# Optimization experiments

Hardware: AMD Instinct MI355X
Metric: run time of the kernel (lower is better)

## Reference

```python
import jax, jax.numpy as jnp
import numpy as np

B, S, D, H, DFF = 4, 2048, 768, 12, 3072
DH = D // H  # 64
EPS = 1e-5
SQRT_DK = float(np.sqrt(DH))


def layer_norm(x, gamma, beta):
    mu = jnp.mean(x, axis=-1, keepdims=True)
    var = jnp.mean((x - mu) ** 2, axis=-1, keepdims=True)
    return (x - mu) / jnp.sqrt(var + EPS) * gamma + beta


def attention_block(x, Wq, Wv, gamma, beta, mask):
    # NOTE: faithful to source quirks: k and v BOTH come from the V projection
    # (self.K is unused), and softmax is over dim=2 (the QUERY axis) as in
    # nn.Softmax(dim=2) applied to a (B, H, Sq, Sk) tensor.
    b, s, d = x.shape
    q = (x @ Wq).reshape(b, s, H, DH).transpose(0, 2, 1, 3)   # (B,H,S,DH)
    kv = (x @ Wv).reshape(b, s, H, DH).transpose(0, 2, 1, 3)  # (B,H,S,DH)
    w = jnp.einsum('bhqd,bhkd->bhqk', q, kv) / SQRT_DK        # (B,H,S,S)
    w = jnp.where(mask, -1e9, w)
    score = jax.nn.softmax(w, axis=2)  # dim=2 quirk (query axis)
    o = jnp.einsum('bhqk,bhkd->bhqd', score, kv)
    o = o.transpose(0, 2, 1, 3).reshape(b, s, d)
    return layer_norm(o + x, gamma, beta)


def feed_forward(x, W1, b1, W2, b2, gamma, beta):
    h = jax.nn.relu(x @ W1 + b1)
    return layer_norm(h @ W2 + b2 + x, gamma, beta)


def setup_inputs() -> dict:
    key = jax.random.key(0)
    ks = jax.random.split(key, 12)
    std = 1.0 / np.sqrt(D)
    x = jax.random.normal(ks[0], (B, S, D), dtype=jnp.float32)
    # causal mask: True = masked
    mask = jnp.triu(jnp.ones((S, S), dtype=bool), k=1)[None, None]
    return {
        'x': x,
        'mask': mask,
        'Wq1': jax.random.normal(ks[1], (D, D), jnp.float32) * std,
        'Wv1': jax.random.normal(ks[2], (D, D), jnp.float32) * std,
        'g1': jnp.ones((D,), jnp.float32),
        'be1': jnp.zeros((D,), jnp.float32),
        'Wq2': jax.random.normal(ks[3], (D, D), jnp.float32) * std,
        'Wv2': jax.random.normal(ks[4], (D, D), jnp.float32) * std,
        'g2': jnp.ones((D,), jnp.float32),
        'be2': jnp.zeros((D,), jnp.float32),
        'Wf1': jax.random.normal(ks[5], (D, DFF), jnp.float32) * std,
        'bf1': jnp.zeros((DFF,), jnp.float32),
        'Wf2': jax.random.normal(ks[6], (DFF, D), jnp.float32) * (1.0 / np.sqrt(DFF)),
        'bf2': jnp.zeros((D,), jnp.float32),
        'gf': jnp.ones((D,), jnp.float32),
        'bef': jnp.zeros((D,), jnp.float32),
    }


def reference(x, mask, Wq1, Wv1, g1, be1, Wq2, Wv2, g2, be2,
              Wf1, bf1, Wf2, bf2, gf, bef):
    x = attention_block(x, Wq1, Wv1, g1, be1, mask)
    # second block: mask is zeroed in the source (no masking)
    x = attention_block(x, Wq2, Wv2, g2, be2, jnp.zeros_like(mask))
    x = feed_forward(x, Wf1, bf1, Wf2, bf2, gf, bef)
    return x
```

## Files before the change

### kernel.cpp

```cpp
#include <hip/hip_runtime.h>

typedef __attribute__((ext_vector_type(8))) short short8;
typedef __attribute__((ext_vector_type(4))) float floatx4;
typedef __attribute__((ext_vector_type(4))) unsigned short ushort4v;

#define H_ 12
#define S_ 2048
#define D_ 768
#define DFF_ 3072
#define DH_ 64
#define BH_ 48
#define M_ 8192

__device__ __forceinline__ unsigned short f2bf(float f) {
  union { float f; unsigned int u; } a; a.f = f;
  return (unsigned short)((a.u + 0x7FFFu + ((a.u >> 16) & 1u)) >> 16);
}

__device__ __forceinline__ void glds16(const void* g, void* l) {
  __builtin_amdgcn_global_load_lds(
      (const __attribute__((address_space(1))) void*)(unsigned long long)(size_t)g,
      (__attribute__((address_space(3))) void*)(unsigned int)(size_t)l, 16, 0, 0);
}
__device__ __forceinline__ void glds4(const void* g, void* l) {
  __builtin_amdgcn_global_load_lds(
      (const __attribute__((address_space(1))) void*)(unsigned long long)(size_t)g,
      (__attribute__((address_space(3))) void*)(unsigned int)(size_t)l, 4, 0, 0);
}

__device__ __forceinline__ int swz8(int lin, int nwg) {
  return (lin & 7) * (nwg >> 3) + (lin >> 3);
}

__global__ __launch_bounds__(256) void cvt_bf16(const float* __restrict__ in,
                                                unsigned short* __restrict__ out) {
  size_t i = ((size_t)blockIdx.x * 256 + threadIdx.x) * 4;
  floatx4 v = *reinterpret_cast<const floatx4*>(in + i);
  ushort4v o;
  o[0] = f2bf(v[0]); o[1] = f2bf(v[1]); o[2] = f2bf(v[2]); o[3] = f2bf(v[3]);
  *reinterpret_cast<ushort4v*>(out + i) = o;
}

__global__ __launch_bounds__(256) void wtrans(const float* __restrict__ W,
                                              unsigned short* __restrict__ Wt,
                                              int K, int N) {
  __shared__ float t[64][65];
  const int n0 = blockIdx.x * 64, k0 = blockIdx.y * 64;
  const int tid = threadIdx.x;
#pragma unroll
  for (int i = 0; i < 16; ++i) {
    int idx = tid + 256 * i;
    int kl = idx >> 6, nl = idx & 63;
    t[kl][nl] = W[(size_t)(k0 + kl) * N + n0 + nl];
  }
  __syncthreads();
#pragma unroll
  for (int i = 0; i < 16; ++i) {
    int idx = tid + 256 * i;
    int nl = idx >> 6, kl = idx & 63;
    Wt[(size_t)(n0 + nl) * K + k0 + kl] = f2bf(t[kl][nl]);
  }
}

__global__ __launch_bounds__(256) void kvtrans(const unsigned short* __restrict__ KVb,
                                               unsigned short* __restrict__ KVTb) {
  __shared__ unsigned short t[64][72];
  const int kk0 = blockIdx.x * 64;
  const int bh = blockIdx.y, b = bh / H_, h = bh % H_;
  const size_t xbase = ((size_t)b * S_) * D_ + h * DH_;
  const int tid = threadIdx.x;
#pragma unroll
  for (int i = 0; i < 16; ++i) {
    int idx = tid + 256 * i;
    int kl = idx >> 6, d = idx & 63;
    t[kl][d] = KVb[xbase + (size_t)(kk0 + kl) * D_ + d];
  }
  __syncthreads();
  const size_t tb = (size_t)bh * DH_ * S_;
#pragma unroll
  for (int i = 0; i < 16; ++i) {
    int idx = tid + 256 * i;
    int d = idx >> 6, kl = idx & 63;
    KVTb[tb + (size_t)d * S_ + kk0 + kl] = t[kl][d];
  }
}

template <int EPI, int OUTBF>
__global__ __launch_bounds__(256, 2) void gemm128(const unsigned short* __restrict__ A,
                                                  const unsigned short* __restrict__ Bt,
                                                  const float* __restrict__ bias,
                                                  float scale, void* __restrict__ C0,
                                                  void* __restrict__ C1,
                                                  int M, int N, int K, int lda) {
  __shared__ unsigned short As[128 * 64];
  __shared__ unsigned short Bs[128 * 64];
  const int tid = threadIdx.x;
  const int l = tid & 63, w = tid >> 6;
  const int wm = w >> 1, wn = w & 1;
  const int lrow = l & 15, lk = l >> 4;
  int lin = (blockIdx.z * gridDim.y + blockIdx.y) * gridDim.x + blockIdx.x;
  int nwg = gridDim.x * gridDim.y * gridDim.z;
  int s = swz8(lin, nwg);
  int xt = s % gridDim.x;
  int rest = s / gridDim.x;
  int yt = rest % gridDim.y;
  int zt = rest / gridDim.y;
  const unsigned short* Ao = A + (size_t)zt * K;
  const unsigned short* Bo = Bt + (size_t)zt * K;
  const int m0 = yt * 128, n0 = xt * 128;
  floatx4 acc[4][4] = {};
  for (int k0 = 0; k0 < K; k0 += 64) {
    __syncthreads();
#pragma unroll
    for (int i = 0; i < 4; ++i) {
      int idx = w * 64 + i * 256 + l;
      int row = idx >> 3, c8 = idx & 7;
      int sc = (c8 ^ (row & 7)) << 3;
      glds16(Ao + (size_t)(m0 + row) * lda + k0 + sc, As + (size_t)(w * 64 + i * 256) * 8);
      glds16(Bo + (size_t)(n0 + row) * lda + k0 + sc, Bs + (size_t)(w * 64 + i * 256) * 8);
    }
    __syncthreads();
#pragma unroll
    for (int ks = 0; ks < 2; ++ks) {
      short8 af[4], bfr[4];
#pragma unroll
      for (int f = 0; f < 4; ++f) {
        int ar = wm * 64 + f * 16 + lrow;
        af[f] = *reinterpret_cast<const short8*>(
            &As[ar * 64 + (((ks * 4 + lk) ^ (ar & 7)) << 3)]);
        int br = wn * 64 + f * 16 + lrow;
        bfr[f] = *reinterpret_cast<const short8*>(
            &Bs[br * 64 + (((ks * 4 + lk) ^ (br & 7)) << 3)]);
      }
#pragma unroll
      for (int fm = 0; fm < 4; ++fm)
#pragma unroll
        for (int fn = 0; fn < 4; ++fn)
          acc[fm][fn] =
              __builtin_amdgcn_mfma_f32_16x16x32_bf16(af[fm], bfr[fn], acc[fm][fn], 0, 0, 0);
    }
  }
#pragma unroll
  for (int fm = 0; fm < 4; ++fm) {
#pragma unroll
    for (int fn = 0; fn < 4; ++fn) {
      int col = n0 + wn * 64 + fn * 16 + lrow;
#pragma unroll
      for (int r = 0; r < 4; ++r) {
        int row = m0 + wm * 64 + fm * 16 + lk * 4 + r;
        float v = acc[fm][fn][r];
        if (EPI == 3) {
          if (col < 768)
            ((unsigned short*)C0)[(size_t)row * 768 + col] = f2bf(v * scale);
          else
            ((unsigned short*)C1)[(size_t)row * 768 + col - 768] = f2bf(v);
        } else {
          v = v * scale + ((EPI > 0) ? bias[col] : 0.0f);
          if (EPI == 1) v = fmaxf(v, 0.0f);
          void* Cz = zt ? C1 : C0;
          if (OUTBF) ((unsigned short*)Cz)[(size_t)row * N + col] = f2bf(v);
          else ((float*)Cz)[(size_t)row * N + col] = v;
        }
      }
    }
  }
}

template <bool CAUSAL>
__global__ __launch_bounds__(256, 4) void colsum(const unsigned short* __restrict__ Qb,
                                                 const unsigned short* __restrict__ KVb,
                                                 float* __restrict__ lnl) {
  __shared__ unsigned short kvs[64 * 64];
  __shared__ float lred[4][64];
  const int tid = threadIdx.x;
  const int l = tid & 63, w = tid >> 6;
  const int lrow = l & 15, lk = l >> 4;
  const int sw = swz8(blockIdx.x, 32 * BH_);
  const int bh = sw >> 5, kt = sw & 31;
  const int kk0 = kt * 64;
  const int b = bh / H_, h = bh % H_;
  const size_t xbase = ((size_t)b * S_) * D_ + h * DH_;
#pragma unroll
  for (int i = 0; i < 2; ++i) {
    int idx = w * 64 + i * 256 + l;
    int row = idx >> 3, c8 = idx & 7;
    glds16(KVb + xbase + (size_t)(kk0 + row) * D_ + ((c8 ^ (row & 7)) << 3),
           kvs + (size_t)(w * 64 + i * 256) * 8);
  }
  __syncthreads();
  short8 bkv[4][2];
#pragma unroll
  for (int kkf = 0; kkf < 4; ++kkf)
#pragma unroll
    for (int s = 0; s < 2; ++s) {
      int br = kkf * 16 + lrow;
      bkv[kkf][s] = *reinterpret_cast<const short8*>(
          &kvs[br * 64 + (((s * 4 + lk) ^ (br & 7)) << 3)]);
    }
  float lrun[4] = {0.0f, 0.0f, 0.0f, 0.0f};
  const int qbase = CAUSAL ? kk0 : 0;
  const int ntiles = (S_ - qbase) >> 4;
  for (int t = w; t < ntiles; t += 4) {
    const int q0 = qbase + t * 16;
    const bool maskt = CAUSAL && (q0 < kk0 + 64);
    short8 aq[2];
#pragma unroll
    for (int s = 0; s < 2; ++s)
      aq[s] = *reinterpret_cast<const short8*>(
          &Qb[xbase + (size_t)(q0 + lrow) * D_ + s * 32 + lk * 8]);
#pragma unroll
    for (int kkf = 0; kkf < 4; ++kkf) {
      floatx4 sf = {};
      sf = __builtin_amdgcn_mfma_f32_16x16x32_bf16(aq[0], bkv[kkf][0], sf, 0, 0, 0);
      sf = __builtin_amdgcn_mfma_f32_16x16x32_bf16(aq[1], bkv[kkf][1], sf, 0, 0, 0);
      const int kkg = kk0 + kkf * 16 + lrow;
      float lacc = 0.0f;
      if (maskt) {
#pragma unroll
        for (int r = 0; r < 4; ++r) {
          int qg = q0 + lk * 4 + r;
          lacc += (kkg <= qg) ? __expf(sf[r]) : 0.0f;
        }
      } else {
#pragma unroll
        for (int r = 0; r < 4; ++r) lacc += __expf(sf[r]);
      }
      lrun[kkf] += lacc;
    }
  }
#pragma unroll
  for (int kkf = 0; kkf < 4; ++kkf) {
    float lv = lrun[kkf];
    lv += __shfl_xor(lv, 16, 64);
    lv += __shfl_xor(lv, 32, 64);
    if (l < 16) lred[w][kkf * 16 + l] = lv;
  }
  __syncthreads();
  if (tid < 64) {
    float lv = lred[0][tid] + lred[1][tid] + lred[2][tid] + lred[3][tid];
    lnl[(size_t)bh * S_ + kk0 + tid] = __logf(lv);
  }
}

template <bool CAUSAL>
__global__ __launch_bounds__(256, 3) void attnpv(const unsigned short* __restrict__ Qb,
                                                 const unsigned short* __restrict__ KVb,
                                                 const unsigned short* __restrict__ KVTb,
                                                 const float* __restrict__ lnl,
                                                 float* __restrict__ Opre) {
  __shared__ unsigned short kvs[2][64 * 64];
  __shared__ unsigned short kvts[2][64 * 64];
  __shared__ float slnl[2][4][64];
  __shared__ unsigned short ps[4][32 * 64];
  const int tid = threadIdx.x;
  const int l = tid & 63, w = tid >> 6;
  const int lrow = l & 15, lk = l >> 4;
  const int sw = swz8(blockIdx.x, 16 * BH_);
  const int bh = sw >> 4, qtr = sw & 15;
  const int qt = CAUSAL ? (15 - qtr) : qtr;
  const int q0 = qt * 128;
  const int wr = w * 32;
  const int b = bh / H_, h = bh % H_;
  const size_t xbase = ((size_t)b * S_) * D_ + h * DH_;
  const size_t tbase = (size_t)bh * DH_ * S_;
  const float* lnlb = lnl + (size_t)bh * S_;

  auto STAGE = [&](int buf, int t) {
    const int kk0 = t * 64;
#pragma unroll
    for (int i = 0; i < 2; ++i) {
      int idx = w * 64 + i * 256 + l;
      int row = idx >> 3, c8 = idx & 7;
      int sc = (c8 ^ (row & 7)) << 3;
      glds16(KVb + xbase + (size_t)(kk0 + row) * D_ + sc,
             &kvs[buf][(size_t)(w * 64 + i * 256) * 8]);
      glds16(KVTb + tbase + (size_t)row * S_ + kk0 + sc,
             &kvts[buf][(size_t)(w * 64 + i * 256) * 8]);
    }
    glds4(lnlb + kk0 + l, &slnl[buf][w][0]);
  };

  short8 aq[2][2];
#pragma unroll
  for (int fm = 0; fm < 2; ++fm)
#pragma unroll
    for (int s = 0; s < 2; ++s)
      aq[fm][s] = *reinterpret_cast<const short8*>(
          &Qb[xbase + (size_t)(q0 + wr + fm * 16 + lrow) * D_ + s * 32 + lk * 8]);
  floatx4 ao[2][4] = {};
  const int nkk = CAUSAL ? 2 * (qt + 1) : (S_ / 64);

  STAGE(0, 0);
  int cur = 0;
  for (int t = 0; t < nkk; ++t) {
    const int kk0 = t * 64;
    const bool maskt = CAUSAL && (kk0 + 64 > q0);
    if (t + 1 < nkk) {
      STAGE(cur ^ 1, t + 1);
      __builtin_amdgcn_sched_barrier(0);
      asm volatile("s_waitcnt vmcnt(5)" ::: "memory");
    } else {
      __builtin_amdgcn_sched_barrier(0);
      asm volatile("s_waitcnt vmcnt(0)" ::: "memory");
    }
    __builtin_amdgcn_s_barrier();
    __builtin_amdgcn_sched_barrier(0);
#pragma unroll
    for (int kkf = 0; kkf < 4; ++kkf) {
      const int kkl = kkf * 16 + lrow;
      const int br = kkf * 16 + lrow;
      short8 b0 =
          *reinterpret_cast<const short8*>(&kvs[cur][br * 64 + ((lk ^ (br & 7)) << 3)]);
      short8 b1 =
          *reinterpret_cast<const short8*>(&kvs[cur][br * 64 + (((4 + lk) ^ (br & 7)) << 3)]);
      const float nl = -slnl[cur][w][kkl];
      const int kkg = kk0 + kkl;
#pragma unroll
      for (int fm = 0; fm < 2; ++fm) {
        floatx4 sf = {nl, nl, nl, nl};
        sf = __builtin_amdgcn_mfma_f32_16x16x32_bf16(aq[fm][0], b0, sf, 0, 0, 0);
        sf = __builtin_amdgcn_mfma_f32_16x16x32_bf16(aq[fm][1], b1, sf, 0, 0, 0);
#pragma unroll
        for (int r = 0; r < 4; ++r) {
          int prow = fm * 16 + lk * 4 + r;
          float p;
          if (maskt)
            p = (kkg <= q0 + wr + prow) ? __expf(sf[r]) : 0.0f;
          else
            p = __expf(sf[r]);
          ps[w][prow * 64 + (((kkl >> 3) ^ (prow & 7)) << 3) + (kkl & 7)] = f2bf(p);
        }
      }
    }
    short8 pa[2][2];
#pragma unroll
    for (int fm = 0; fm < 2; ++fm)
#pragma unroll
      for (int s2 = 0; s2 < 2; ++s2)
        pa[fm][s2] = *reinterpret_cast<const short8*>(
            &ps[w][(fm * 16 + lrow) * 64 + (((s2 * 4 + lk) ^ (lrow & 7)) << 3)]);
    __builtin_amdgcn_s_setprio(1);
#pragma unroll
    for (int dn = 0; dn < 4; ++dn) {
#pragma unroll
      for (int s2 = 0; s2 < 2; ++s2) {
        const int br2 = dn * 16 + lrow;
        short8 bv = *reinterpret_cast<const short8*>(
            &kvts[cur][br2 * 64 + (((s2 * 4 + lk) ^ (br2 & 7)) << 3)]);
#pragma unroll
        for (int fm = 0; fm < 2; ++fm)
          ao[fm][dn] =
              __builtin_amdgcn_mfma_f32_16x16x32_bf16(pa[fm][s2], bv, ao[fm][dn], 0, 0, 0);
      }
    }
    __builtin_amdgcn_s_setprio(0);
    __builtin_amdgcn_sched_barrier(0);
    __builtin_amdgcn_s_barrier();
    __builtin_amdgcn_sched_barrier(0);
    cur ^= 1;
  }
#pragma unroll
  for (int fm = 0; fm < 2; ++fm)
#pragma unroll
    for (int dn = 0; dn < 4; ++dn)
#pragma unroll
      for (int r = 0; r < 4; ++r)
        Opre[xbase + (size_t)(q0 + wr + fm * 16 + lk * 4 + r) * D_ + dn * 16 + lrow] =
            ao[fm][dn][r];
}

template <bool WRITEBF, bool TWO, bool BIAS>
__global__ __launch_bounds__(256) void ln_kernel(const float* __restrict__ pre,
                                                 const float* __restrict__ pre2,
                                                 const float* __restrict__ bias,
                                                 const float* __restrict__ res,
                                                 const float* __restrict__ gam,
                                                 const float* __restrict__ bet,
                                                 float* __restrict__ outf,
                                                 unsigned short* __restrict__ outb) {
  __shared__ float red[8];
  const int tid = threadIdx.x;
  const size_t base = (size_t)blockIdx.x * D_;
  float v[3];
  float s = 0.0f;
#pragma unroll
  for (int j = 0; j < 3; ++j) {
    int i = tid + 256 * j;
    float t = pre[base + i] + res[base + i];
    if (TWO) t += pre2[base + i];
    if (BIAS) t += bias[i];
    v[j] = t;
    s += t;
  }
#pragma unroll
  for (int off = 32; off; off >>= 1) s += __shfl_xor(s, off, 64);
  if ((tid & 63) == 0) red[tid >> 6] = s;
  __syncthreads();
  s = red[0] + red[1] + red[2] + red[3];
  const float mu = s * (1.0f / 768.0f);
  float vs = 0.0f;
#pragma unroll
  for (int j = 0; j < 3; ++j) { float d = v[j] - mu; vs += d * d; }
#pragma unroll
  for (int off = 32; off; off >>= 1) vs += __shfl_xor(vs, off, 64);
  if ((tid & 63) == 0) red[4 + (tid >> 6)] = vs;
  __syncthreads();
  vs = red[4] + red[5] + red[6] + red[7];
  const float rstd = rsqrtf(vs * (1.0f / 768.0f) + 1e-5f);
#pragma unroll
  for (int j = 0; j < 3; ++j) {
    int i = tid + 256 * j;
    float o = (v[j] - mu) * rstd * gam[i] + bet[i];
    outf[base + i] = o;
    if (WRITEBF) outb[base + i] = f2bf(o);
  }
}

extern "C" void kernel_launch(void* const* d_in, const int* in_sizes, int n_in,
                              void* d_out, int out_size, void* d_ws, size_t ws_size,
                              hipStream_t stream) {
  const float* x = (const float*)d_in[0];
  const float* Wq1 = (const float*)d_in[2];
  const float* Wv1 = (const float*)d_in[3];
  const float* g1 = (const float*)d_in[4];
  const float* be1 = (const float*)d_in[5];
  const float* Wq2 = (const float*)d_in[6];
  const float* Wv2 = (const float*)d_in[7];
  const float* g2 = (const float*)d_in[8];
  const float* be2 = (const float*)d_in[9];
  const float* Wf1 = (const float*)d_in[10];
  const float* bf1 = (const float*)d_in[11];
  const float* Wf2 = (const float*)d_in[12];
  const float* bf2 = (const float*)d_in[13];
  const float* gf = (const float*)d_in[14];
  const float* bef = (const float*)d_in[15];

  char* ws = (char*)d_ws;
  size_t off = 0;
  auto alloc = [&](size_t bytes) -> void* {
    void* p = ws + off;
    off += (bytes + 255) & ~(size_t)255;
    return p;
  };
  unsigned short* xb = (unsigned short*)alloc((size_t)M_ * D_ * 2);
  unsigned short* qb = (unsigned short*)alloc((size_t)M_ * D_ * 2);
  unsigned short* kvb = (unsigned short*)alloc((size_t)M_ * D_ * 2);
  unsigned short* kvtb = (unsigned short*)alloc((size_t)BH_ * DH_ * S_ * 2);
  float* lnl = (float*)alloc((size_t)BH_ * S_ * 4);
  float* preA = (float*)alloc((size_t)M_ * D_ * 4);
  float* xcur = (float*)alloc((size_t)M_ * D_ * 4);
  unsigned short* hb = (unsigned short*)alloc((size_t)M_ * DFF_ * 2);
  unsigned short* wqv1t = (unsigned short*)alloc((size_t)D_ * 1536 * 2);
  unsigned short* wqv2t = (unsigned short*)alloc((size_t)D_ * 1536 * 2);
  unsigned short* wf1t = (unsigned short*)alloc((size_t)D_ * DFF_ * 2);
  unsigned short* wf2t = (unsigned short*)alloc((size_t)D_ * DFF_ * 2);
  float* preB = (float*)qb;
  if (off > ws_size) return;

  const dim3 blk(256);
  cvt_bf16<<<dim3((M_ * D_) / 1024), blk, 0, stream>>>(x, xb);
  wtrans<<<dim3(12, 12), blk, 0, stream>>>(Wq1, wqv1t, D_, D_);
  wtrans<<<dim3(12, 12), blk, 0, stream>>>(Wv1, wqv1t + (size_t)768 * 768, D_, D_);
  wtrans<<<dim3(12, 12), blk, 0, stream>>>(Wq2, wqv2t, D_, D_);
  wtrans<<<dim3(12, 12), blk, 0, stream>>>(Wv2, wqv2t + (size_t)768 * 768, D_, D_);
  wtrans<<<dim3(48, 12), blk, 0, stream>>>(Wf1, wf1t, D_, DFF_);
  wtrans<<<dim3(12, 48), blk, 0, stream>>>(Wf2, wf2t, DFF_, D_);

  const dim3 gqkv(12, 64);
  const dim3 gkvt(S_ / 64, BH_);

  gemm128<3, 1><<<gqkv, blk, 0, stream>>>(xb, wqv1t, nullptr, 0.125f, qb, kvb, M_, 1536, D_, D_);
  kvtrans<<<gkvt, blk, 0, stream>>>(kvb, kvtb);
  colsum<true><<<dim3(32 * BH_), blk, 0, stream>>>(qb, kvb, lnl);
  attnpv<true><<<dim3(16 * BH_), blk, 0, stream>>>(qb, kvb, kvtb, lnl, preA);
  ln_kernel<true, false, false><<<dim3(M_), blk, 0, stream>>>(preA, nullptr, nullptr, x, g1,
                                                              be1, xcur, xb);

  gemm128<3, 1><<<gqkv, blk, 0, stream>>>(xb, wqv2t, nullptr, 0.125f, qb, kvb, M_, 1536, D_, D_);
  kvtrans<<<gkvt, blk, 0, stream>>>(kvb, kvtb);
  colsum<false><<<dim3(32 * BH_), blk, 0, stream>>>(qb, kvb, lnl);
  attnpv<false><<<dim3(16 * BH_), blk, 0, stream>>>(qb, kvb, kvtb, lnl, preA);
  ln_kernel<true, false, false><<<dim3(M_), blk, 0, stream>>>(preA, nullptr, nullptr, xcur, g2,
                                                              be2, xcur, xb);

  gemm128<1, 1><<<dim3(24, 64), blk, 0, stream>>>(xb, wf1t, bf1, 1.0f, hb, nullptr, M_, DFF_,
                                                  D_, D_);
  gemm128<0, 0><<<dim3(6, 64, 2), blk, 0, stream>>>(hb, wf2t, nullptr, 1.0f, preA, preB, M_, D_,
                                                    DFF_ / 2, DFF_);
  ln_kernel<false, true, true><<<dim3(M_), blk, 0, stream>>>(preA, preB, bf2, xcur, gf, bef,
                                                             (float*)d_out, nullptr);
}
```

Baseline: 516.8 us.

## Use exp2 softmax with folded log2e, packed bf16 P stores, prefetch Q, one-wave LayerNorm

The Q scale now folds in log2(e) so the softmax kernels use exp2 and log2 hardware intrinsics instead of expf and logf. The stored log normalizer is negated, so attnpv can load it as a float4 accumulator init. attnpv swaps the MFMA operand order so each lane holds four consecutive keys, which lets the P tile be written to LDS with packed v_cvt_pk_bf16 32-bit stores. colsum software-prefetches the next Q tile. LayerNorm is rewritten to one wavefront per row with float4 loads and no LDS or barriers.

```diff
diff --git a/kernel.cpp b/kernel.cpp
--- a/kernel.cpp
+++ b/kernel.cpp
@@ -11,10 +11,31 @@
 #define DH_ 64
 #define BH_ 48
 #define M_ 8192
+#define QSCALE 0.180336880f
+
+#if defined(__has_builtin)
+#if __has_builtin(__builtin_amdgcn_exp2f)
+#define EXP2V(x) __builtin_amdgcn_exp2f(x)
+#endif
+#if __has_builtin(__builtin_amdgcn_logf)
+#define LOG2V(x) __builtin_amdgcn_logf(x)
+#endif
+#endif
+#ifndef EXP2V
+#define EXP2V(x) exp2f(x)
+#endif
+#ifndef LOG2V
+#define LOG2V(x) log2f(x)
+#endif
 
 __device__ __forceinline__ unsigned short f2bf(float f) {
   union { float f; unsigned int u; } a; a.f = f;
   return (unsigned short)((a.u + 0x7FFFu + ((a.u >> 16) & 1u)) >> 16);
+}
+__device__ __forceinline__ unsigned int cvtpk_bf16(float lo, float hi) {
+  unsigned int u;
+  asm("v_cvt_pk_bf16_f32 %0, %1, %2" : "=v"(u) : "v"(lo), "v"(hi));
+  return u;
 }
 
 __device__ __forceinline__ void glds16(const void* g, void* l) {
@@ -200,30 +221,41 @@
   float lrun[4] = {0.0f, 0.0f, 0.0f, 0.0f};
   const int qbase = CAUSAL ? kk0 : 0;
   const int ntiles = (S_ - qbase) >> 4;
+  short8 aqn[2];
+  if (w < ntiles) {
+    const int q0 = qbase + w * 16;
+#pragma unroll
+    for (int s = 0; s < 2; ++s)
+      aqn[s] = *reinterpret_cast<const short8*>(
+          &Qb[xbase + (size_t)(q0 + lrow) * D_ + s * 32 + lk * 8]);
+  }
   for (int t = w; t < ntiles; t += 4) {
     const int q0 = qbase + t * 16;
     const bool maskt = CAUSAL && (q0 < kk0 + 64);
-    short8 aq[2];
-#pragma unroll
-    for (int s = 0; s < 2; ++s)
-      aq[s] = *reinterpret_cast<const short8*>(
-          &Qb[xbase + (size_t)(q0 + lrow) * D_ + s * 32 + lk * 8]);
+    short8 aq0 = aqn[0], aq1 = aqn[1];
+    if (t + 4 < ntiles) {
+      const int qn = qbase + (t + 4) * 16;
+#pragma unroll
+      for (int s = 0; s < 2; ++s)
+        aqn[s] = *reinterpret_cast<const short8*>(
+            &Qb[xbase + (size_t)(qn + lrow) * D_ + s * 32 + lk * 8]);
+    }
 #pragma unroll
     for (int kkf = 0; kkf < 4; ++kkf) {
       floatx4 sf = {};
-      sf = __builtin_amdgcn_mfma_f32_16x16x32_bf16(aq[0], bkv[kkf][0], sf, 0, 0, 0);
-      sf = __builtin_amdgcn_mfma_f32_16x16x32_bf16(aq[1], bkv[kkf][1], sf, 0, 0, 0);
+      sf = __builtin_amdgcn_mfma_f32_16x16x32_bf16(aq0, bkv[kkf][0], sf, 0, 0, 0);
+      sf = __builtin_amdgcn_mfma_f32_16x16x32_bf16(aq1, bkv[kkf][1], sf, 0, 0, 0);
       const int kkg = kk0 + kkf * 16 + lrow;
       float lacc = 0.0f;
       if (maskt) {
 #pragma unroll
         for (int r = 0; r < 4; ++r) {
           int qg = q0 + lk * 4 + r;
-          lacc += (kkg <= qg) ? __expf(sf[r]) : 0.0f;
+          lacc += (kkg <= qg) ? EXP2V(sf[r]) : 0.0f;
         }
       } else {
 #pragma unroll
-        for (int r = 0; r < 4; ++r) lacc += __expf(sf[r]);
+        for (int r = 0; r < 4; ++r) lacc += EXP2V(sf[r]);
       }
       lrun[kkf] += lacc;
     }
@@ -238,7 +270,7 @@
   __syncthreads();
   if (tid < 64) {
     float lv = lred[0][tid] + lred[1][tid] + lred[2][tid] + lred[3][tid];
-    lnl[(size_t)bh * S_ + kk0 + tid] = __logf(lv);
+    lnl[(size_t)bh * S_ + kk0 + tid] = -LOG2V(lv);
   }
 }
 
@@ -307,29 +339,38 @@
     __builtin_amdgcn_sched_barrier(0);
 #pragma unroll
     for (int kkf = 0; kkf < 4; ++kkf) {
-      const int kkl = kkf * 16 + lrow;
       const int br = kkf * 16 + lrow;
       short8 b0 =
           *reinterpret_cast<const short8*>(&kvs[cur][br * 64 + ((lk ^ (br & 7)) << 3)]);
       short8 b1 =
           *reinterpret_cast<const short8*>(&kvs[cur][br * 64 + (((4 + lk) ^ (br & 7)) << 3)]);
-      const float nl = -slnl[cur][w][kkl];
-      const int kkg = kk0 + kkl;
+      const floatx4 nl4 =
+          *reinterpret_cast<const floatx4*>(&slnl[cur][w][kkf * 16 + lk * 4]);
+      const int kkbase = kk0 + kkf * 16 + lk * 4;
 #pragma unroll
       for (int fm = 0; fm < 2; ++fm) {
-        floatx4 sf = {nl, nl, nl, nl};
-        sf = __builtin_amdgcn_mfma_f32_16x16x32_bf16(aq[fm][0], b0, sf, 0, 0, 0);
-        sf = __builtin_amdgcn_mfma_f32_16x16x32_bf16(aq[fm][1], b1, sf, 0, 0, 0);
-#pragma unroll
-        for (int r = 0; r < 4; ++r) {
-          int prow = fm * 16 + lk * 4 + r;
-          float p;
-          if (maskt)
-            p = (kkg <= q0 + wr + prow) ? __expf(sf[r]) : 0.0f;
-          else
-            p = __expf(sf[r]);
-          ps[w][prow * 64 + (((kkl >> 3) ^ (prow & 7)) << 3) + (kkl & 7)] = f2bf(p);
+        floatx4 sf = nl4;
+        sf = __builtin_amdgcn_mfma_f32_16x16x32_bf16(b0, aq[fm][0], sf, 0, 0, 0);
+        sf = __builtin_amdgcn_mfma_f32_16x16x32_bf16(b1, aq[fm][1], sf, 0, 0, 0);
+        float p0 = EXP2V(sf[0]);
+        float p1 = EXP2V(sf[1]);
+        float p2 = EXP2V(sf[2]);
+        float p3 = EXP2V(sf[3]);
+        if (maskt) {
+          const int qg = q0 + wr + fm * 16 + lrow;
+          p0 = (kkbase + 0 <= qg) ? p0 : 0.0f;
+          p1 = (kkbase + 1 <= qg) ? p1 : 0.0f;
+          p2 = (kkbase + 2 <= qg) ? p2 : 0.0f;
+          p3 = (kkbase + 3 <= qg) ? p3 : 0.0f;
         }
+        unsigned int u0 = cvtpk_bf16(p0, p1);
+        unsigned int u1 = cvtpk_bf16(p2, p3);
+        const int rowq = fm * 16 + lrow;
+        unsigned short* pb =
+            &ps[w][rowq * 64 + ((((kkf << 1) + (lk >> 1)) ^ (lrow & 7)) << 3) +
+                   ((lk & 1) << 2)];
+        *reinterpret_cast<unsigned int*>(pb) = u0;
+        *reinterpret_cast<unsigned int*>(pb + 2) = u1;
       }
     }
     short8 pa[2][2];
@@ -378,41 +419,58 @@
                                                  const float* __restrict__ bet,
                                                  float* __restrict__ outf,
                                                  unsigned short* __restrict__ outb) {
-  __shared__ float red[8];
-  const int tid = threadIdx.x;
-  const size_t base = (size_t)blockIdx.x * D_;
-  float v[3];
+  const int w = threadIdx.x >> 6, l = threadIdx.x & 63;
+  const int row = blockIdx.x * 4 + w;
+  const size_t base = (size_t)row * D_;
+  floatx4 v[3];
   float s = 0.0f;
 #pragma unroll
   for (int j = 0; j < 3; ++j) {
-    int i = tid + 256 * j;
-    float t = pre[base + i] + res[base + i];
-    if (TWO) t += pre2[base + i];
-    if (BIAS) t += bias[i];
+    int i = j * 256 + l * 4;
+    floatx4 t = *reinterpret_cast<const floatx4*>(&pre[base + i]);
+    floatx4 rv = *reinterpret_cast<const floatx4*>(&res[base + i]);
+#pragma unroll
+    for (int e = 0; e < 4; ++e) t[e] += rv[e];
+    if (TWO) {
+      floatx4 t2 = *reinterpret_cast<const floatx4*>(&pre2[base + i]);
+#pragma unroll
+      for (int e = 0; e < 4; ++e) t[e] += t2[e];
+    }
+    if (BIAS) {
+      floatx4 bv = *reinterpret_cast<const floatx4*>(&bias[i]);
+#pragma unroll
+      for (int e = 0; e < 4; ++e) t[e] += bv[e];
+    }
     v[j] = t;
-    s += t;
+#pragma unroll
+    for (int e = 0; e < 4; ++e) s += t[e];
   }
 #pragma unroll
   for (int off = 32; off; off >>= 1) s += __shfl_xor(s, off, 64);
-  if ((tid & 63) == 0) red[tid >> 6] = s;
-  __syncthreads();
-  s = red[0] + red[1] + red[2] + red[3];
   const float mu = s * (1.0f / 768.0f);
   float vs = 0.0f;
 #pragma unroll
-  for (int j = 0; j < 3; ++j) { float d = v[j] - mu; vs += d * d; }
+  for (int j = 0; j < 3; ++j)
+#pragma unroll
+    for (int e = 0; e < 4; ++e) { float d = v[j][e] - mu; vs += d * d; }
 #pragma unroll
   for (int off = 32; off; off >>= 1) vs += __shfl_xor(vs, off, 64);
-  if ((tid & 63) == 0) red[4 + (tid >> 6)] = vs;
-  __syncthreads();
-  vs = red[4] + red[5] + red[6] + red[7];
   const float rstd = rsqrtf(vs * (1.0f / 768.0f) + 1e-5f);
 #pragma unroll
   for (int j = 0; j < 3; ++j) {
-    int i = tid + 256 * j;
-    float o = (v[j] - mu) * rstd * gam[i] + bet[i];
-    outf[base + i] = o;
-    if (WRITEBF) outb[base + i] = f2bf(o);
+    int i = j * 256 + l * 4;
+    floatx4 gv = *reinterpret_cast<const floatx4*>(&gam[i]);
+    floatx4 bev = *reinterpret_cast<const floatx4*>(&bet[i]);
+    floatx4 o;
+#pragma unroll
+    for (int e = 0; e < 4; ++e) o[e] = (v[j][e] - mu) * rstd * gv[e] + bev[e];
+    *reinterpret_cast<floatx4*>(&outf[base + i]) = o;
+    if (WRITEBF) {
+      ushort4v ob;
+#pragma unroll
+      for (int e = 0; e < 4; ++e) ob[e] = f2bf(o[e]);
+      *reinterpret_cast<ushort4v*>(&outb[base + i]) = ob;
+    }
   }
 }
 
@@ -469,24 +527,24 @@
   const dim3 gqkv(12, 64);
   const dim3 gkvt(S_ / 64, BH_);
 
-  gemm128<3, 1><<<gqkv, blk, 0, stream>>>(xb, wqv1t, nullptr, 0.125f, qb, kvb, M_, 1536, D_, D_);
+  gemm128<3, 1><<<gqkv, blk, 0, stream>>>(xb, wqv1t, nullptr, QSCALE, qb, kvb, M_, 1536, D_, D_);
   kvtrans<<<gkvt, blk, 0, stream>>>(kvb, kvtb);
   colsum<true><<<dim3(32 * BH_), blk, 0, stream>>>(qb, kvb, lnl);
   attnpv<true><<<dim3(16 * BH_), blk, 0, stream>>>(qb, kvb, kvtb, lnl, preA);
-  ln_kernel<true, false, false><<<dim3(M_), blk, 0, stream>>>(preA, nullptr, nullptr, x, g1,
-                                                              be1, xcur, xb);
-
-  gemm128<3, 1><<<gqkv, blk, 0, stream>>>(xb, wqv2t, nullptr, 0.125f, qb, kvb, M_, 1536, D_, D_);
+  ln_kernel<true, false, false><<<dim3(M_ / 4), blk, 0, stream>>>(preA, nullptr, nullptr, x, g1,
+                                                                  be1, xcur, xb);
+
+  gemm128<3, 1><<<gqkv, blk, 0, stream>>>(xb, wqv2t, nullptr, QSCALE, qb, kvb, M_, 1536, D_, D_);
   kvtrans<<<gkvt, blk, 0, stream>>>(kvb, kvtb);
   colsum<false><<<dim3(32 * BH_), blk, 0, stream>>>(qb, kvb, lnl);
   attnpv<false><<<dim3(16 * BH_), blk, 0, stream>>>(qb, kvb, kvtb, lnl, preA);
-  ln_kernel<true, false, false><<<dim3(M_), blk, 0, stream>>>(preA, nullptr, nullptr, xcur, g2,
-                                                              be2, xcur, xb);
+  ln_kernel<true, false, false><<<dim3(M_ / 4), blk, 0, stream>>>(preA, nullptr, nullptr, xcur,
+                                                                  g2, be2, xcur, xb);
 
   gemm128<1, 1><<<dim3(24, 64), blk, 0, stream>>>(xb, wf1t, bf1, 1.0f, hb, nullptr, M_, DFF_,
                                                   D_, D_);
   gemm128<0, 0><<<dim3(6, 64, 2), blk, 0, stream>>>(hb, wf2t, nullptr, 1.0f, preA, preB, M_, D_,
                                                     DFF_ / 2, DFF_);
-  ln_kernel<false, true, true><<<dim3(M_), blk, 0, stream>>>(preA, preB, bf2, xcur, gf, bef,
-                                                             (float*)d_out, nullptr);
-}
+  ln_kernel<false, true, true><<<dim3(M_ / 4), blk, 0, stream>>>(preA, preB, bf2, xcur, gf, bef,
+                                                                 (float*)d_out, nullptr);
+}
```

Result: faster. 468.7 us (-9.3%).
